# Optimization experiments

Hardware: AMD Instinct MI355X
Metric: run time of the kernel (lower is better)

Reference implementation:

```python
import jax, jax.numpy as jnp
import numpy as np
import itertools

B = 2; DIM = 256; HEADS = 8; RES = 256; WIN = 16
FWS = WIN // 2            # freq window size = 8
HD = DIM // HEADS         # head dim = 32
N = FWS * FWS             # tokens per window = 64
SCALE = HD ** -0.5

def _make_bias_idxs():
    pts = list(itertools.product(range(FWS), range(FWS)))
    offs, idxs = {}, []
    for p1 in pts:
        for p2 in pts:
            o = (abs(p1[0] - p2[0]), abs(p1[1] - p2[1]))
            if o not in offs:
                offs[o] = len(offs)
            idxs.append(offs[o])
    return np.asarray(idxs, np.int32).reshape(N, N), len(offs)

def _conv(x, w, stride, pad, groups, lhs_dilation=None):
    return jax.lax.conv_general_dilated(
        x, w, (stride, stride), pad, lhs_dilation=lhs_dilation,
        feature_group_count=groups, dimension_numbers=('NCHW', 'OIHW', 'NCHW'))

def _window_partition(x, ws):
    b, c, h, w = x.shape
    x = x.reshape(b, c, h // ws, ws, w // ws, ws)
    x = x.transpose(0, 2, 4, 1, 3, 5)
    return x.reshape(-1, c, ws, ws)

def _window_reverse(x, ws, h, w):
    nh, nw = h // ws, w // ws
    c = x.shape[1]
    x = x.reshape(-1, nh, nw, c, ws, ws)
    x = x.transpose(0, 3, 1, 4, 2, 5)
    return x.reshape(-1, c, h, w)

def setup_inputs():
    key = jax.random.key(0)
    ks = jax.random.split(key, 8)
    idxs, n_off = _make_bias_idxs()
    return {
        'x': jax.random.normal(ks[0], (B, DIM, RES, RES), jnp.float32),
        'wt_filter': jax.random.normal(ks[1], (4 * DIM, 1, 2, 2), jnp.float32) * 0.1,
        'iwt_filter': jax.random.normal(ks[2], (4 * DIM, 1, 2, 2), jnp.float32) * 0.1,
        'dw_weight': jax.random.normal(ks[3], (HEADS, HD, 1, 5, 5), jnp.float32) * 0.1,
        'dw_bias': jax.random.normal(ks[4], (HEADS, HD), jnp.float32) * 0.1,
        'proj_weight': jax.random.normal(ks[5], (DIM, DIM), jnp.float32) * 0.05,
        'proj_bias': jax.random.normal(ks[6], (DIM,), jnp.float32) * 0.1,
        'attention_biases': jax.random.normal(ks[7], (HEADS, n_off), jnp.float32) * 0.1,
        'bias_idxs': jnp.asarray(idxs),
    }

def reference(x, wt_filter, iwt_filter, dw_weight, dw_bias, proj_weight, proj_bias, attention_biases, bias_idxs):
    b, c, h, w = x.shape
    h2, w2 = h // 2, w // 2
    # DWT: grouped stride-2 conv producing 4 subbands per channel (k=2 -> pad 0)
    xw = _conv(x, wt_filter, 2, 'VALID', c).reshape(b, c, 4, h2, w2)
    ll, lh, hl, hh = xw[:, :, 0], xw[:, :, 1], xw[:, :, 2], xw[:, :, 3]
    llw = _window_partition(ll, FWS)   # (Bn, C, 8, 8)
    lhw = _window_partition(lh, FWS)
    hlw = _window_partition(hl, FWS)
    bn = llw.shape[0]
    bias = attention_biases[:, bias_idxs]  # (HEADS, N, N) relative-pos bias gather
    outs = []
    ll_i = llw[:, :HD]
    for i in range(HEADS):  # sequential over heads: ll_i accumulates
        sl = slice(i * HD, (i + 1) * HD)
        if i > 0:
            ll_i = ll_i + llw[:, sl]
        # per-head depthwise 5x5 conv (BN folded) as Q projection of LH band
        q = _conv(lhw[:, sl], dw_weight[i], 1, ((2, 2), (2, 2)), HD) \
            + dw_bias[i][None, :, None, None]
        q = q.reshape(bn, HD, N).transpose(0, 2, 1)        # (Bn, N, hd)
        k = hlw[:, sl].reshape(bn, HD, N)                  # (Bn, hd, N)
        v = ll_i.reshape(bn, HD, N)                        # (Bn, hd, N)
        attn = jnp.einsum('bnd,bdm->bnm', q, k) * SCALE + bias[i]
        attn = jax.nn.softmax(attn, axis=-1)
        ll_i = jnp.einsum('bdm,bnm->bdn', v, attn).reshape(bn, HD, FWS, FWS)
        outs.append(ll_i)
    ll_out = jnp.concatenate(outs, axis=1)
    # proj: ReLU -> 1x1 conv with BN folded into weight/bias
    ll_out = jnp.einsum('oc,bchw->bohw', proj_weight, jax.nn.relu(ll_out)) \
             + proj_bias[None, :, None, None]
    ll_out = _window_reverse(ll_out, FWS, h2, w2)
    wt_out = jnp.stack([ll_out, lh, hl, hh], axis=2).reshape(b, 4 * c, h2, w2)
    # IDWT: conv_transpose(stride=2, pad=0) == input-dilated conv, flipped kernel
    kT = iwt_filter.reshape(c, 4, 2, 2)[:, :, ::-1, ::-1]
    return _conv(wt_out, kT, 1, ((1, 1), (1, 1)), c, lhs_dilation=(2, 2))
```

## Files before the change

kernel.cpp:

```cpp
#include <hip/hip_runtime.h>
#include <hip/hip_bf16.h>

typedef __hip_bfloat16 bf16;

__device__ __forceinline__ float b2f(bf16 v) { return __bfloat162float(v); }
__device__ __forceinline__ bf16 f2b(float v) { return __float2bfloat16(v); }
__device__ __forceinline__ float us2f(unsigned short u) {
  return __uint_as_float(((unsigned)u) << 16);
}
__device__ __forceinline__ void up2(unsigned u, float& lo, float& hi) {
  lo = __uint_as_float(u << 16);
  hi = __uint_as_float(u & 0xFFFF0000u);
}

__device__ __forceinline__ bool detect_f32(const void* p) {
  const unsigned* u = (const unsigned*)p;
  int c = 0;
#pragma unroll
  for (int i = 0; i < 64; ++i) {
    unsigned e = (u[i] >> 7) & 0xFF;
    c += (e >= 170);
  }
  return c > 0;
}

__device__ __forceinline__ float ldp(const void* p, int i, bool f32) {
  return f32 ? ((const float*)p)[i] : b2f(((const bf16*)p)[i]);
}
__device__ __forceinline__ void ldpair(const void* p, size_t du, bool f32,
                                       float& a, float& b) {
  if (f32) {
    float2 v = ((const float2*)p)[du];
    a = v.x; b = v.y;
  } else {
    up2(((const unsigned*)p)[du], a, b);
  }
}

#define SCALE 0.17677669529663687f

__global__ __launch_bounds__(256, 2) void fused_kernel(
    const void* __restrict__ x, const void* __restrict__ wtf,
    const void* __restrict__ iwtf,
    const void* __restrict__ dww, const void* __restrict__ dwb,
    const void* __restrict__ pw, const void* __restrict__ pb,
    const void* __restrict__ ab, const int* __restrict__ bidx,
    void* __restrict__ out) {
  __shared__ float lh_s[32 * 65];
  __shared__ float k_s[32 * 65];
  __shared__ float v_s[32 * 65];
  __shared__ float out_s[32 * 68];
  __shared__ float q_s[64 * 33];
  __shared__ __align__(16) char un_pool[16896];
  __shared__ float w5_s[800];
  __shared__ float wf_s[512];
  __shared__ float ab_s[64];
  float* attn_s = (float*)un_pool;
  unsigned short* pw_su = (unsigned short*)un_pool;

  const bool xf = detect_f32(x);
  const bool pf = detect_f32(pw);

  int t = threadIdx.x;
  int w = blockIdx.x;
  int b = w >> 8, wi = w & 255, wy = wi >> 4, wx = wi & 15;

  float acc[8][8] = {};
  int to = t >> 3, tp = t & 7;

#pragma unroll 1
  for (int h = 0; h < 8; ++h) {
    wf_s[t] = ldp(wtf, h * 512 + t, pf);
    wf_s[t + 256] = ldp(wtf, h * 512 + 256 + t, pf);
#pragma unroll
    for (int e = 0; e < 4; ++e) {
      int idx = t + 256 * e;
      if (idx < 800) w5_s[idx] = ldp(dww, h * 800 + idx, pf);
    }
    if (t < 64) ab_s[t] = ldp(ab, h * 64 + t, pf);
    __syncthreads();

#pragma unroll
    for (int e = 0; e < 8; ++e) {
      int idx = t + 256 * e;
      int d = idx >> 6, p = idx & 63;
      int r = p >> 3, cc = p & 7;
      int plane = b * 256 + h * 32 + d;
      int row = wy * 16 + 2 * r;
      size_t du = ((size_t)plane << 15) + (row << 7) + wx * 8 + cc;
      float x00, x01, x10, x11;
      ldpair(x, du, xf, x00, x01);
      ldpair(x, du + 128, xf, x10, x11);
      const float* f = wf_s + d * 16;
      float llv = x00 * f[0] + x01 * f[1] + x10 * f[2] + x11 * f[3];
      lh_s[d * 65 + p] = x00 * f[4] + x01 * f[5] + x10 * f[6] + x11 * f[7];
      k_s[d * 65 + p]  = x00 * f[8] + x01 * f[9] + x10 * f[10] + x11 * f[11];
      if (h == 0)
        v_s[d * 65 + p] = llv;
      else
        v_s[d * 65 + p] = out_s[d * 68 + p] + llv;
    }
    __syncthreads();

#pragma unroll
    for (int e = 0; e < 8; ++e) {
      int idx = t + 256 * e;
      int d = idx & 31, n = idx >> 5;
      int r = n >> 3, cc = n & 7;
      float qa = ldp(dwb, h * 32 + d, pf);
      for (int u = 0; u < 5; ++u) {
        int rr = r + u - 2;
        if (rr < 0 || rr > 7) continue;
        for (int v = 0; v < 5; ++v) {
          int c2 = cc + v - 2;
          if (c2 < 0 || c2 > 7) continue;
          qa += lh_s[d * 65 + rr * 8 + c2] * w5_s[d * 25 + u * 5 + v];
        }
      }
      q_s[n * 33 + d] = qa;
    }
    __syncthreads();

    {
      int m = t & 63, ng = t >> 6;
      float kreg[32];
#pragma unroll
      for (int d = 0; d < 32; ++d) kreg[d] = k_s[d * 65 + m];
#pragma unroll
      for (int nn = 0; nn < 16; ++nn) {
        int n = ng * 16 + nn;
        float a2 = 0.f;
#pragma unroll
        for (int d = 0; d < 32; ++d) a2 += q_s[n * 33 + d] * kreg[d];
        attn_s[n * 65 + m] = a2 * SCALE + ab_s[bidx[n * 64 + m]];
      }
    }
    __syncthreads();

    if (t < 64) {
      float mx = -1e30f;
      for (int mm = 0; mm < 64; ++mm) mx = fmaxf(mx, attn_s[t * 65 + mm]);
      float s = 0.f;
      for (int mm = 0; mm < 64; ++mm) {
        float e2 = __expf(attn_s[t * 65 + mm] - mx);
        attn_s[t * 65 + mm] = e2;
        s += e2;
      }
      float inv = 1.f / s;
      for (int mm = 0; mm < 64; ++mm) attn_s[t * 65 + mm] *= inv;
    }
    __syncthreads();

    {
      int d = t & 31, n0 = (t >> 5) * 8;
      float pv[8] = {0, 0, 0, 0, 0, 0, 0, 0};
      for (int mm = 0; mm < 64; ++mm) {
        float vv = v_s[d * 65 + mm];
#pragma unroll
        for (int e = 0; e < 8; ++e) pv[e] += vv * attn_s[(n0 + e) * 65 + mm];
      }
#pragma unroll
      for (int e = 0; e < 8; ++e) out_s[d * 68 + n0 + e] = pv[e];
    }
    __syncthreads();

    {
      unsigned short* dst = pw_su + t * 33;
#pragma unroll
      for (int e = 0; e < 32; ++e) {
        float wv = ldp(pw, t * 256 + h * 32 + e, pf);
        dst[e] = (unsigned short)(__float_as_uint(wv) >> 16);
      }
    }
    __syncthreads();

    for (int kk = 0; kk < 32; ++kk) {
      float r[8];
#pragma unroll
      for (int pi = 0; pi < 8; ++pi)
        r[pi] = fmaxf(out_s[kk * 68 + tp + 8 * pi], 0.f);
#pragma unroll
      for (int i2 = 0; i2 < 8; ++i2) {
        float wv = us2f(pw_su[(to + 32 * i2) * 33 + kk]);
#pragma unroll
        for (int pi = 0; pi < 8; ++pi) acc[i2][pi] += wv * r[pi];
      }
    }
    __syncthreads();
  }

#pragma unroll 1
  for (int i2 = 0; i2 < 8; ++i2) {
    int o = to + 32 * i2;
    float pbv = ldp(pb, o, pf);
    float f[16], g[16];
#pragma unroll
    for (int e = 0; e < 16; ++e) {
      f[e] = ldp(wtf, o * 16 + e, pf);
      g[e] = ldp(iwtf, o * 16 + e, pf);
    }
    int plane = b * 256 + o;
#pragma unroll
    for (int pi = 0; pi < 8; ++pi) {
      int y = wy * 8 + pi;
      int xb = wx * 8 + tp;
      float llv = acc[i2][pi] + pbv;
      size_t du = ((size_t)plane << 15) + ((size_t)(2 * y) << 7) + xb;
      float x00, x01, x10, x11;
      ldpair(x, du, xf, x00, x01);
      ldpair(x, du + 128, xf, x10, x11);
      float lhv = x00 * f[4] + x01 * f[5] + x10 * f[6] + x11 * f[7];
      float hlv = x00 * f[8] + x01 * f[9] + x10 * f[10] + x11 * f[11];
      float hhv = x00 * f[12] + x01 * f[13] + x10 * f[14] + x11 * f[15];
#pragma unroll
      for (int sy = 0; sy < 2; ++sy) {
        float v0 = llv * g[0 + sy * 2] + lhv * g[4 + sy * 2] +
                   hlv * g[8 + sy * 2] + hhv * g[12 + sy * 2];
        float v1 = llv * g[1 + sy * 2] + lhv * g[5 + sy * 2] +
                   hlv * g[9 + sy * 2] + hhv * g[13 + sy * 2];
        size_t oi = ((size_t)plane << 15) + ((size_t)(2 * y + sy) << 7) + xb;
        if (xf) {
          ((float2*)out)[oi] = make_float2(v0, v1);
        } else {
          union { bf16 hh2[2]; unsigned u; } pk;
          pk.hh2[0] = f2b(v0);
          pk.hh2[1] = f2b(v1);
          ((unsigned*)out)[oi] = pk.u;
        }
      }
    }
  }
}

extern "C" void kernel_launch(void* const* d_in, const int* in_sizes, int n_in,
                              void* d_out, int out_size, void* d_ws, size_t ws_size,
                              hipStream_t stream) {
  const void *x, *wtf, *iwtf, *dww, *dwb, *pw, *pb, *ab;
  const int* bidx;
  if (in_sizes[0] == 33554432) {
    x = d_in[0]; wtf = d_in[1]; iwtf = d_in[2]; dww = d_in[3]; dwb = d_in[4];
    pw = d_in[5]; pb = d_in[6]; ab = d_in[7]; bidx = (const int*)d_in[8];
  } else if (in_sizes[0] == 512) {
    ab = d_in[0]; bidx = (const int*)d_in[1]; dwb = d_in[2]; dww = d_in[3];
    iwtf = d_in[4]; pb = d_in[5]; pw = d_in[6]; wtf = d_in[7]; x = d_in[8];
  } else {
    bidx = (const int*)d_in[0]; ab = d_in[1]; pb = d_in[2]; pw = d_in[3];
    dwb = d_in[4]; dww = d_in[5]; iwtf = d_in[6]; wtf = d_in[7]; x = d_in[8];
  }

  fused_kernel<<<512, 256, 0, stream>>>(x, wtf, iwtf, dww, dwb, pw, pb, ab,
                                        bidx, d_out);
}
```

Baseline: 615.6 us.

## Prefetch next head's inputs, fuse softmax via wave shuffles, stream proj weights

The x tile and the per-head filter weights for the next head are now prefetched into registers while the current head is processed, which hides global-load latency behind compute. Softmax is fused into the QK pass using 64-lane shuffle reductions, and normalisation is deferred to the PV output. This removes the serial 64-thread softmax stage and one barrier. Projection weights are read directly from global memory as float4 instead of being staged in shared memory as truncated bf16, which drops two barriers but adds register pressure and more global reads. Block indices are also swizzled and bias indices are hoisted into registers.

After: 745.3 us. +21.1%, slower.

```diff
diff --git a/kernel.cpp b/kernel.cpp
--- a/kernel.cpp
+++ b/kernel.cpp
@@ -5,9 +5,6 @@
 
 __device__ __forceinline__ float b2f(bf16 v) { return __bfloat162float(v); }
 __device__ __forceinline__ bf16 f2b(float v) { return __float2bfloat16(v); }
-__device__ __forceinline__ float us2f(unsigned short u) {
-  return __uint_as_float(((unsigned)u) << 16);
-}
 __device__ __forceinline__ void up2(unsigned u, float& lo, float& hi) {
   lo = __uint_as_float(u << 16);
   hi = __uint_as_float(u & 0xFFFF0000u);
@@ -34,6 +31,16 @@
     a = v.x; b = v.y;
   } else {
     up2(((const unsigned*)p)[du], a, b);
+  }
+}
+__device__ __forceinline__ void ld4(const void* p, size_t i, bool f32,
+                                    float4& o) {
+  if (f32) {
+    o = ((const float4*)p)[i >> 2];
+  } else {
+    uint2 u = ((const uint2*)p)[i >> 2];
+    up2(u.x, o.x, o.y);
+    up2(u.y, o.z, o.w);
   }
 }
 
@@ -51,78 +58,118 @@
   __shared__ float v_s[32 * 65];
   __shared__ float out_s[32 * 68];
   __shared__ float q_s[64 * 33];
-  __shared__ __align__(16) char un_pool[16896];
+  __shared__ float attn_s[64 * 65];
   __shared__ float w5_s[800];
   __shared__ float wf_s[512];
   __shared__ float ab_s[64];
-  float* attn_s = (float*)un_pool;
-  unsigned short* pw_su = (unsigned short*)un_pool;
+  __shared__ float inv_s[64];
 
   const bool xf = detect_f32(x);
   const bool pf = detect_f32(pw);
 
   int t = threadIdx.x;
-  int w = blockIdx.x;
+  int w = ((blockIdx.x & 7) << 6) | (blockIdx.x >> 3);
   int b = w >> 8, wi = w & 255, wy = wi >> 4, wx = wi & 15;
 
   float acc[8][8] = {};
   int to = t >> 3, tp = t & 7;
+  int m = t & 63, ng = t >> 6;
+
+  int bidx_r[16];
+#pragma unroll
+  for (int nn = 0; nn < 16; ++nn) bidx_r[nn] = bidx[(ng * 16 + nn) * 64 + m];
+
+  float X0[8], X1[8], X2[8], X3[8];
+#pragma unroll
+  for (int e = 0; e < 8; ++e) {
+    int idx = t + 256 * e;
+    int d = idx >> 6, p = idx & 63, r = p >> 3, cc = p & 7;
+    int plane = b * 256 + d;
+    size_t du = ((size_t)plane << 15) + ((wy * 16 + 2 * r) << 7) + wx * 8 + cc;
+    ldpair(x, du, xf, X0[e], X1[e]);
+    ldpair(x, du + 128, xf, X2[e], X3[e]);
+  }
+  float pwf0 = ldp(wtf, t, pf), pwf1 = ldp(wtf, 256 + t, pf);
+  float pw5r[4];
+#pragma unroll
+  for (int e2 = 0; e2 < 4; ++e2) {
+    int idx = t + 256 * e2;
+    pw5r[e2] = (idx < 800) ? ldp(dww, idx, pf) : 0.f;
+  }
+  float pabr = (t < 64) ? ldp(ab, t, pf) : 0.f;
 
 #pragma unroll 1
   for (int h = 0; h < 8; ++h) {
-    wf_s[t] = ldp(wtf, h * 512 + t, pf);
-    wf_s[t + 256] = ldp(wtf, h * 512 + 256 + t, pf);
-#pragma unroll
-    for (int e = 0; e < 4; ++e) {
-      int idx = t + 256 * e;
-      if (idx < 800) w5_s[idx] = ldp(dww, h * 800 + idx, pf);
-    }
-    if (t < 64) ab_s[t] = ldp(ab, h * 64 + t, pf);
+    wf_s[t] = pwf0;
+    wf_s[t + 256] = pwf1;
+#pragma unroll
+    for (int e2 = 0; e2 < 4; ++e2) {
+      int idx = t + 256 * e2;
+      if (idx < 800) w5_s[idx] = pw5r[e2];
+    }
+    if (t < 64) ab_s[t] = pabr;
+    if (h < 7) {
+      pwf0 = ldp(wtf, (h + 1) * 512 + t, pf);
+      pwf1 = ldp(wtf, (h + 1) * 512 + 256 + t, pf);
+#pragma unroll
+      for (int e2 = 0; e2 < 4; ++e2) {
+        int idx = t + 256 * e2;
+        if (idx < 800) pw5r[e2] = ldp(dww, (h + 1) * 800 + idx, pf);
+      }
+      if (t < 64) pabr = ldp(ab, (h + 1) * 64 + t, pf);
+    }
     __syncthreads();
 
 #pragma unroll
     for (int e = 0; e < 8; ++e) {
       int idx = t + 256 * e;
       int d = idx >> 6, p = idx & 63;
-      int r = p >> 3, cc = p & 7;
-      int plane = b * 256 + h * 32 + d;
-      int row = wy * 16 + 2 * r;
-      size_t du = ((size_t)plane << 15) + (row << 7) + wx * 8 + cc;
-      float x00, x01, x10, x11;
-      ldpair(x, du, xf, x00, x01);
-      ldpair(x, du + 128, xf, x10, x11);
       const float* f = wf_s + d * 16;
-      float llv = x00 * f[0] + x01 * f[1] + x10 * f[2] + x11 * f[3];
-      lh_s[d * 65 + p] = x00 * f[4] + x01 * f[5] + x10 * f[6] + x11 * f[7];
-      k_s[d * 65 + p]  = x00 * f[8] + x01 * f[9] + x10 * f[10] + x11 * f[11];
+      float llv = X0[e] * f[0] + X1[e] * f[1] + X2[e] * f[2] + X3[e] * f[3];
+      lh_s[d * 65 + p] = X0[e] * f[4] + X1[e] * f[5] + X2[e] * f[6] + X3[e] * f[7];
+      k_s[d * 65 + p] = X0[e] * f[8] + X1[e] * f[9] + X2[e] * f[10] + X3[e] * f[11];
       if (h == 0)
         v_s[d * 65 + p] = llv;
       else
         v_s[d * 65 + p] = out_s[d * 68 + p] + llv;
     }
-    __syncthreads();
-
-#pragma unroll
-    for (int e = 0; e < 8; ++e) {
-      int idx = t + 256 * e;
-      int d = idx & 31, n = idx >> 5;
-      int r = n >> 3, cc = n & 7;
-      float qa = ldp(dwb, h * 32 + d, pf);
-      for (int u = 0; u < 5; ++u) {
-        int rr = r + u - 2;
-        if (rr < 0 || rr > 7) continue;
-        for (int v = 0; v < 5; ++v) {
-          int c2 = cc + v - 2;
-          if (c2 < 0 || c2 > 7) continue;
-          qa += lh_s[d * 65 + rr * 8 + c2] * w5_s[d * 25 + u * 5 + v];
+    if (h < 7) {
+#pragma unroll
+      for (int e = 0; e < 8; ++e) {
+        int idx = t + 256 * e;
+        int d = idx >> 6, p = idx & 63, r = p >> 3, cc = p & 7;
+        int plane = b * 256 + (h + 1) * 32 + d;
+        size_t du =
+            ((size_t)plane << 15) + ((wy * 16 + 2 * r) << 7) + wx * 8 + cc;
+        ldpair(x, du, xf, X0[e], X1[e]);
+        ldpair(x, du + 128, xf, X2[e], X3[e]);
+      }
+    }
+    __syncthreads();
+
+    {
+      float dwbv = ldp(dwb, h * 32 + (t & 31), pf);
+#pragma unroll
+      for (int e = 0; e < 8; ++e) {
+        int idx = t + 256 * e;
+        int d = idx & 31, n = idx >> 5;
+        int r = n >> 3, cc = n & 7;
+        float qa = dwbv;
+        for (int u = 0; u < 5; ++u) {
+          int rr = r + u - 2;
+          if (rr < 0 || rr > 7) continue;
+          for (int v = 0; v < 5; ++v) {
+            int c2 = cc + v - 2;
+            if (c2 < 0 || c2 > 7) continue;
+            qa += lh_s[d * 65 + rr * 8 + c2] * w5_s[d * 25 + u * 5 + v];
+          }
         }
-      }
-      q_s[n * 33 + d] = qa;
+        q_s[n * 33 + d] = qa;
+      }
     }
     __syncthreads();
 
     {
-      int m = t & 63, ng = t >> 6;
       float kreg[32];
 #pragma unroll
       for (int d = 0; d < 32; ++d) kreg[d] = k_s[d * 65 + m];
@@ -132,22 +179,18 @@
         float a2 = 0.f;
 #pragma unroll
         for (int d = 0; d < 32; ++d) a2 += q_s[n * 33 + d] * kreg[d];
-        attn_s[n * 65 + m] = a2 * SCALE + ab_s[bidx[n * 64 + m]];
-      }
-    }
-    __syncthreads();
-
-    if (t < 64) {
-      float mx = -1e30f;
-      for (int mm = 0; mm < 64; ++mm) mx = fmaxf(mx, attn_s[t * 65 + mm]);
-      float s = 0.f;
-      for (int mm = 0; mm < 64; ++mm) {
-        float e2 = __expf(attn_s[t * 65 + mm] - mx);
-        attn_s[t * 65 + mm] = e2;
-        s += e2;
-      }
-      float inv = 1.f / s;
-      for (int mm = 0; mm < 64; ++mm) attn_s[t * 65 + mm] *= inv;
+        a2 = a2 * SCALE + ab_s[bidx_r[nn]];
+        float mx = a2;
+#pragma unroll
+        for (int msk = 32; msk > 0; msk >>= 1)
+          mx = fmaxf(mx, __shfl_xor(mx, msk, 64));
+        float e2 = __expf(a2 - mx);
+        float sum = e2;
+#pragma unroll
+        for (int msk = 32; msk > 0; msk >>= 1) sum += __shfl_xor(sum, msk, 64);
+        attn_s[n * 65 + m] = e2;
+        if (m == 0) inv_s[n] = 1.f / sum;
+      }
     }
     __syncthreads();
 
@@ -160,33 +203,35 @@
         for (int e = 0; e < 8; ++e) pv[e] += vv * attn_s[(n0 + e) * 65 + mm];
       }
 #pragma unroll
-      for (int e = 0; e < 8; ++e) out_s[d * 68 + n0 + e] = pv[e];
-    }
-    __syncthreads();
-
-    {
-      unsigned short* dst = pw_su + t * 33;
-#pragma unroll
-      for (int e = 0; e < 32; ++e) {
-        float wv = ldp(pw, t * 256 + h * 32 + e, pf);
-        dst[e] = (unsigned short)(__float_as_uint(wv) >> 16);
-      }
-    }
-    __syncthreads();
-
-    for (int kk = 0; kk < 32; ++kk) {
-      float r[8];
-#pragma unroll
-      for (int pi = 0; pi < 8; ++pi)
-        r[pi] = fmaxf(out_s[kk * 68 + tp + 8 * pi], 0.f);
-#pragma unroll
-      for (int i2 = 0; i2 < 8; ++i2) {
-        float wv = us2f(pw_su[(to + 32 * i2) * 33 + kk]);
-#pragma unroll
-        for (int pi = 0; pi < 8; ++pi) acc[i2][pi] += wv * r[pi];
-      }
-    }
-    __syncthreads();
+      for (int e = 0; e < 8; ++e)
+        out_s[d * 68 + n0 + e] = pv[e] * inv_s[n0 + e];
+    }
+    __syncthreads();
+
+#pragma unroll 1
+    for (int q4 = 0; q4 < 8; ++q4) {
+      float4 w4[8];
+#pragma unroll
+      for (int i2 = 0; i2 < 8; ++i2)
+        ld4(pw, (size_t)(to + 32 * i2) * 256 + h * 32 + q4 * 4, pf, w4[i2]);
+#pragma unroll
+      for (int j = 0; j < 4; ++j) {
+        int kk = q4 * 4 + j;
+        float r[8];
+#pragma unroll
+        for (int pi = 0; pi < 8; ++pi)
+          r[pi] = fmaxf(out_s[kk * 68 + tp + 8 * pi], 0.f);
+#pragma unroll
+        for (int i2 = 0; i2 < 8; ++i2) {
+          float wv = (j == 0)   ? w4[i2].x
+                     : (j == 1) ? w4[i2].y
+                     : (j == 2) ? w4[i2].z
+                                : w4[i2].w;
+#pragma unroll
+          for (int pi = 0; pi < 8; ++pi) acc[i2][pi] += wv * r[pi];
+        }
+      }
+    }
   }
 
 #pragma unroll 1
```
